# Performance work log

Measured on AMD Instinct MI355X. Metric: run time of the kernel, lower is better.

## Reference

```python
import jax, jax.numpy as jnp
import numpy as np
import math

B, T, D = 2, 2048, 1024
H, HD = 16, 64          # num_heads, head_dim = D // H
ROPE, BASE = 64, 10000.0  # rope covers full head dim
GLOBAL_IDS = jnp.array([2, 3, 4, 5, 6, 7], dtype=jnp.int32)


def setup_inputs() -> dict:
    key = jax.random.key(0)
    k1, k2, k3, k4 = jax.random.split(key, 4)
    x = jax.random.normal(k1, (B, T, D), dtype=jnp.float32)
    input_ids = jax.random.randint(k2, (B, T), 0, 1024, dtype=jnp.int32)
    W_qkv = jax.random.normal(k3, (3 * H * HD, D), dtype=jnp.float32) * 0.02
    b_qkv = jnp.zeros((3 * H * HD,), dtype=jnp.float32)
    W_out = jax.random.normal(k4, (D, H * HD), dtype=jnp.float32) * 0.02
    b_out = jnp.zeros((D,), dtype=jnp.float32)
    return {"x": x, "input_ids": input_ids, "W_qkv": W_qkv, "b_qkv": b_qkv,
            "W_out": W_out, "b_out": b_out}


def _apply_rotary(x, cos, sin):
    # x: [B,H,T,HD]; rope covers first ROPE dims (= full head here)
    x_rot, x_pass = x[..., :ROPE], x[..., ROPE:]
    half = ROPE // 2
    x1, x2 = x_rot[..., :half], x_rot[..., half:]
    x1n = x1 * cos - x2 * sin
    x2n = x1 * sin + x2 * cos
    return jnp.concatenate([x1n, x2n, x_pass], axis=-1)


def reference(x, input_ids, W_qkv, b_qkv, W_out, b_out):
    Bx, Tx, _ = x.shape
    qkv = x @ W_qkv.T + b_qkv                      # [B,T,3*H*HD]
    q, k, v = jnp.split(qkv, 3, axis=-1)
    def heads(t):
        return t.reshape(Bx, Tx, H, HD).transpose(0, 2, 1, 3)  # [B,H,T,HD]
    q, k, v = heads(q), heads(k), heads(v)

    # RoPE
    pos = jnp.arange(Tx, dtype=jnp.float32)
    inv_freq = 1.0 / (BASE ** (jnp.arange(0, ROPE, 2, dtype=jnp.float32) / ROPE))
    freqs = pos[:, None] * inv_freq[None, :]        # [T, ROPE//2]
    cos, sin = jnp.cos(freqs)[None, None], jnp.sin(freqs)[None, None]
    q = _apply_rotary(q, cos, sin)
    k = _apply_rotary(k, cos, sin)

    # causal mask OR global-query rows (BigBird-style)
    causal = jnp.tril(jnp.ones((Tx, Tx), dtype=bool))[None, None]   # [1,1,T,T]
    global_mask = jnp.isin(input_ids, GLOBAL_IDS)                    # [B,T]
    allow = causal | global_mask[:, None, :, None]                   # [B,1,T,T]

    scale = math.sqrt(HD)
    logits = jnp.einsum('bhqd,bhkd->bhqk', q, k) / scale
    neg = -jnp.finfo(logits.dtype).max
    logits = jnp.where(allow, logits, neg)
    attn = jax.nn.softmax(logits, axis=-1)
    out = jnp.einsum('bhqk,bhkd->bhqd', attn, v)
    out = out.transpose(0, 2, 1, 3).reshape(Bx, Tx, H * HD)
    return out @ W_out.T + b_out
```

## Files before the change

### kernel.cpp

```cpp
#include <hip/hip_runtime.h>
#include <math.h>

#define Bc 2
#define Tc 2048
#define Dc 1024
#define Hc 16
#define HDc 64

typedef __attribute__((ext_vector_type(8))) short bf16x8;
typedef __attribute__((ext_vector_type(4))) float f32x4;
typedef __attribute__((ext_vector_type(16))) float f32x16;

__device__ __forceinline__ unsigned short f2bf(float f) {
    union { float f; unsigned int u; } v; v.f = f;
    unsigned int r = (v.u + 0x7FFFu + ((v.u >> 16) & 1u)) >> 16;
    return (unsigned short)r;
}
__device__ __forceinline__ unsigned pack2bf(float a, float b) {
    unsigned au = __float_as_uint(a) + 0x8000u;
    unsigned bu = __float_as_uint(b) + 0x8000u;
    return __builtin_amdgcn_perm(bu, au, 0x07060302u);
}

__device__ __forceinline__ void gload_lds16(const unsigned short* g,
                                            unsigned short* l) {
    __builtin_amdgcn_global_load_lds(
        (const __attribute__((address_space(1))) unsigned int*)g,
        (__attribute__((address_space(3))) unsigned int*)l,
        16, 0, 0);
}

#define CEXP 0.1803368801111204f

__global__ __launch_bounds__(256) void convert_bf16(
    const float* __restrict__ x, const float* __restrict__ wqkv,
    const float* __restrict__ wout,
    unsigned short* __restrict__ xb, unsigned short* __restrict__ wqkvb,
    unsigned short* __restrict__ woutb, float2* __restrict__ ropeTab)
{
    const int gid = blockIdx.x * 256 + threadIdx.x;
    if (gid < Tc * 32) {
        const int t = gid >> 5, i = gid & 31;
        const float freq = exp2f((float)i * -0.4152410118609203f);
        const float ang = (float)t * freq;
        ropeTab[gid] = make_float2(cosf(ang), sinf(ang));
    }
#pragma unroll
    for (int it = 0; it < 4; it++) {
        const int i = (it * 524288 + gid) * 4;
        const float* src; unsigned short* dst; int off;
        if (i < 4194304)      { src = x;    dst = xb;    off = i; }
        else if (i < 7340032) { src = wqkv; dst = wqkvb; off = i - 4194304; }
        else                  { src = wout; dst = woutb; off = i - 7340032; }
        float4 v = *(const float4*)&src[off];
        ushort4 o;
        o.x = f2bf(v.x); o.y = f2bf(v.y); o.z = f2bf(v.z); o.w = f2bf(v.w);
        *(ushort4*)&dst[off] = o;
    }
}

template <int MODE, int MT, int NT>
__global__ __launch_bounds__(256) void gemm_mfma(
    const unsigned short* __restrict__ A, const unsigned short* __restrict__ W,
    const float* __restrict__ bias, float* __restrict__ C,
    unsigned short* __restrict__ Qp, unsigned short* __restrict__ Kp,
    unsigned short* __restrict__ Vtp, const float2* __restrict__ ropeTab,
    int M, int N, int K)
{
    __shared__ unsigned short Apk[MT * 32 * 64];
    __shared__ unsigned short Bpk[NT * 32 * 64];

    const int tid = threadIdx.x;
    const int lane = tid & 63;
    const int wave = tid >> 6;
    const int quad = lane >> 4;
    const int c = lane & 15;
    const int wm = wave >> 1;
    const int wn = wave & 1;

    const int flat = blockIdx.y * gridDim.x + blockIdx.x;
    const int cpx = gridDim.x >> 3;
    const int xcd = flat & 7;
    const int idxq = flat >> 3;
    const int bx = xcd * cpx + (idxq % cpx);
    const int by = idxq / cpx;
    const int m0 = by * (MT * 32);
    const int n0 = bx * (NT * 32);

    f32x4 acc[MT][NT];
#pragma unroll
    for (int mt = 0; mt < MT; mt++)
#pragma unroll
        for (int nt = 0; nt < NT; nt++) acc[mt][nt] = (f32x4){0.f, 0.f, 0.f, 0.f};

    const int lrow = lane >> 3;
    const int srcoct = (lane & 7) ^ lrow;

    for (int k0 = 0; k0 < K; k0 += 64) {
        __syncthreads();
#pragma unroll
        for (int i = 0; i < MT; i++) {
            const int r = wave * (MT * 8) + i * 8 + lrow;
            gload_lds16(&A[(size_t)(m0 + r) * K + k0 + srcoct * 8],
                        &Apk[(wave * MT * 8 + i * 8) * 64]);
        }
#pragma unroll
        for (int i = 0; i < NT; i++) {
            const int r = wave * (NT * 8) + i * 8 + lrow;
            gload_lds16(&W[(size_t)(n0 + r) * K + k0 + srcoct * 8],
                        &Bpk[(wave * NT * 8 + i * 8) * 64]);
        }
        __syncthreads();
#pragma unroll
        for (int ko = 0; ko < 2; ko++) {
            bf16x8 af[MT], bf[NT];
#pragma unroll
            for (int mt = 0; mt < MT; mt++) {
                const int m = wm * (MT * 16) + mt * 16 + c;
                af[mt] = *(const bf16x8*)&Apk[(m * 8 + ((ko * 4 + quad) ^ (m & 7))) * 8];
            }
#pragma unroll
            for (int nt = 0; nt < NT; nt++) {
                const int n = wn * (NT * 16) + nt * 16 + c;
                bf[nt] = *(const bf16x8*)&Bpk[(n * 8 + ((ko * 4 + quad) ^ (n & 7))) * 8];
            }
#pragma unroll
            for (int mt = 0; mt < MT; mt++)
#pragma unroll
                for (int nt = 0; nt < NT; nt++)
                    acc[mt][nt] = __builtin_amdgcn_mfma_f32_16x16x32_bf16(
                        af[mt], bf[nt], acc[mt][nt], 0, 0, 0);
        }
    }

    if (MODE == 0) {
#pragma unroll
        for (int mt = 0; mt < MT; mt++) {
            const int m = m0 + wm * (MT * 16) + mt * 16 + quad * 4;
#pragma unroll
            for (int nt = 0; nt < NT; nt++) {
                const int n = n0 + wn * (NT * 16) + nt * 16 + c;
                const float bv = bias[n];
#pragma unroll
                for (int reg = 0; reg < 4; reg++)
                    C[(size_t)(m + reg) * N + n] = acc[mt][nt][reg] + bv;
            }
        }
    } else {
        const int n_wave = n0 + wn * 64;
        const int which = n_wave >> 10;
        const int h = (n_wave >> 6) & 15;
        const int b = m0 >> 11;
        const int t_base = (m0 & 2047) + wm * 64;

        __syncthreads();
        unsigned short* stg = ((wave < 2) ? Apk : Bpk) + (wave & 1) * 4096;

        if (which < 2) {
            unsigned short* dst = (which == 0) ? Qp : Kp;
#pragma unroll
            for (int mt = 0; mt < 4; mt++) {
#pragma unroll
                for (int nt = 0; nt < 2; nt++) {
                    const int i1 = nt * 16 + c;
                    const float bv1 = bias[n_wave + i1];
                    const float bv2 = bias[n_wave + 32 + i1];
#pragma unroll
                    for (int reg = 0; reg < 4; reg++) {
                        const int row = mt * 16 + quad * 4 + reg;
                        const float2 cs = ropeTab[(t_base + row) * 32 + i1];
                        const float x1 = acc[mt][nt][reg] + bv1;
                        const float x2 = acc[mt][nt + 2][reg] + bv2;
                        const int col2 = 32 + i1;
                        stg[(row * 8 + ((i1 >> 3) ^ (row & 7))) * 8 + (i1 & 7)] =
                            f2bf(x1 * cs.x - x2 * cs.y);
                        stg[(row * 8 + ((col2 >> 3) ^ (row & 7))) * 8 + (col2 & 7)] =
                            f2bf(x1 * cs.y + x2 * cs.x);
                    }
                }
            }
            const size_t obase = ((size_t)(b * Hc + h) * Tc + t_base) * HDc;
            const int oct = lane & 7;
#pragma unroll
            for (int k = 0; k < 8; k++) {
                const int f = lane * 8 + k * 512;
                const int row = f >> 6;
                bf16x8 vv = *(const bf16x8*)&stg[(row * 8 + (oct ^ (row & 7))) * 8];
                *(bf16x8*)&dst[obase + f] = vv;
            }
        } else {
#pragma unroll
            for (int mt = 0; mt < 4; mt++) {
#pragma unroll
                for (int nt = 0; nt < 4; nt++) {
                    const int d = nt * 16 + c;
                    const float bv = bias[n_wave + d];
#pragma unroll
                    for (int reg = 0; reg < 4; reg++) {
                        const int r = mt * 16 + quad * 4 + reg;
                        stg[(d * 8 + ((r >> 3) ^ (d & 7))) * 8 + (r & 7)] =
                            f2bf(acc[mt][nt][reg] + bv);
                    }
                }
            }
            const size_t vbase = (size_t)(b * Hc + h) * HDc * Tc;
            const int oct = lane & 7;
#pragma unroll
            for (int k = 0; k < 8; k++) {
                const int d = (lane >> 3) + k * 8;
                bf16x8 vv = *(const bf16x8*)&stg[(d * 8 + (oct ^ (d & 7))) * 8];
                *(bf16x8*)&Vtp[vbase + (size_t)d * Tc + t_base + oct * 8] = vv;
            }
        }
    }
}

__global__ __launch_bounds__(256, 4) void attn_fused(
    const unsigned short* __restrict__ Q, const unsigned short* __restrict__ K,
    const unsigned short* __restrict__ Vt, const int* __restrict__ ids,
    unsigned short* __restrict__ AO)
{
    __shared__ __align__(16) float smem[8448];

    const int tid = threadIdx.x;
    const int lane = tid & 63;
    const int wave = tid >> 6;
    const int c32 = lane & 31;
    const int h = lane >> 5;
    const int blk = blockIdx.x;

    if (blk < 32) {
        int* s_list = (int*)smem;
        int* s_cnt = (int*)smem + 64;
        float* s_accm = smem + 128;
        float* s_lm = s_accm + 8192;

        const int bh = blk;
        const int b = bh >> 4;
        const int hd = bh & 15;
        const size_t qkbase = (size_t)bh * Tc * HDc;

        if (tid == 0) *s_cnt = 0;
        __syncthreads();
        for (int i = tid; i < Tc; i += 256) {
            int id = ids[b * Tc + i];
            if ((unsigned)(id - 2) <= 5u) {
                int p = atomicAdd(s_cnt, 1);
                if (p < 64) s_list[p] = i;
            }
        }
        __syncthreads();
        const int cnt = min(*s_cnt, 64);

        for (int pass = 0; pass * 32 < cnt; pass++) {
            const int slot = pass * 32 + c32;
            const int row = (slot < cnt) ? s_list[slot] : s_list[0];

            bf16x8 qf[4];
#pragma unroll
            for (int ko = 0; ko < 4; ko++)
                qf[ko] = *(const bf16x8*)&Q[qkbase + (size_t)row * HDc + ko * 16 + h * 8];

            f32x16 acc0 = {}, acc1 = {};
            float lacc = 0.0f;

            for (int it = wave; it < Tc / 64; it += 4) {
                const int t0 = it * 64;
                f32x16 s0 = {}, s1 = {};
#pragma unroll
                for (int ko = 0; ko < 4; ko++) {
                    const int koff = ko * 16 + h * 8;
                    bf16x8 kf0 = *(const bf16x8*)&K[qkbase + (size_t)(t0 + c32) * HDc + koff];
                    bf16x8 kf1 = *(const bf16x8*)&K[qkbase + (size_t)(t0 + 32 + c32) * HDc + koff];
                    s0 = __builtin_amdgcn_mfma_f32_32x32x16_bf16(kf0, qf[ko], s0, 0, 0, 0);
                    s1 = __builtin_amdgcn_mfma_f32_32x32x16_bf16(kf1, qf[ko], s1, 0, 0, 0);
                }
                float v[32];
#pragma unroll
                for (int r = 0; r < 16; r++) { v[r] = s0[r]; v[16 + r] = s1[r]; }
#pragma unroll
                for (int i = 0; i < 32; i++) v[i] = exp2f(v[i] * CEXP);
                unsigned pk[16];
#pragma unroll
                for (int i = 0; i < 16; i++) pk[i] = pack2bf(v[2 * i], v[2 * i + 1]);
#pragma unroll
                for (int st = 1; st < 32; st <<= 1)
#pragma unroll
                    for (int i = 0; i < 32; i += 2 * st) v[i] += v[i + st];
                lacc += v[0];
#pragma unroll
                for (int ko = 0; ko < 4; ko++) {
                    const int a = (ko >> 1) * 8 + (ko & 1) * 4;
                    unsigned keep0 = h ? pk[a + 2] : pk[a + 0];
                    unsigned keep1 = h ? pk[a + 3] : pk[a + 1];
                    unsigned send0 = h ? pk[a + 0] : pk[a + 2];
                    unsigned send1 = h ? pk[a + 1] : pk[a + 3];
                    unsigned recv0 = (unsigned)__shfl_xor((int)send0, 32);
                    unsigned recv1 = (unsigned)__shfl_xor((int)send1, 32);
                    union { bf16x8 v8; unsigned u[4]; } pf;
                    pf.u[0] = h ? recv0 : keep0;
                    pf.u[1] = h ? recv1 : keep1;
                    pf.u[2] = h ? keep0 : recv0;
                    pf.u[3] = h ? keep1 : recv1;
                    const int oct = ko * 2 + h;
                    bf16x8 vf0 = *(const bf16x8*)&Vt[qkbase + (size_t)c32 * Tc + t0 + oct * 8];
                    bf16x8 vf1 = *(const bf16x8*)&Vt[qkbase + (size_t)(32 + c32) * Tc + t0 + oct * 8];
                    acc0 = __builtin_amdgcn_mfma_f32_32x32x16_bf16(vf0, pf.v8, acc0, 0, 0, 0);
                    acc1 = __builtin_amdgcn_mfma_f32_32x32x16_bf16(vf1, pf.v8, acc1, 0, 0, 0);
                }
            }

            const float lfull = lacc + __shfl_xor(lacc, 32);
            if (h == 0) s_lm[wave * 32 + c32] = lfull;
#pragma unroll
            for (int r = 0; r < 16; r++) {
                const int d = (r & 3) + 8 * (r >> 2) + 4 * h;
                s_accm[(wave * 64 + d) * 32 + c32] = acc0[r];
                s_accm[(wave * 64 + 32 + d) * 32 + c32] = acc1[r];
            }
            __syncthreads();
            for (int i = tid; i < 2048; i += 256) {
                const int sl = i >> 6, d = i & 63;
                if (pass * 32 + sl < cnt) {
                    const float o = s_accm[(0 * 64 + d) * 32 + sl] + s_accm[(1 * 64 + d) * 32 + sl] +
                                    s_accm[(2 * 64 + d) * 32 + sl] + s_accm[(3 * 64 + d) * 32 + sl];
                    const float lt = s_lm[sl] + s_lm[32 + sl] + s_lm[64 + sl] + s_lm[96 + sl];
                    const int qrow = s_list[pass * 32 + sl];
                    AO[((size_t)(b * Tc + qrow)) * Dc + hd * HDc + d] = f2bf(o / lt);
                }
            }
            __syncthreads();
        }
        return;
    }

    unsigned short* KV = (unsigned short*)smem;
    unsigned short* Ke = KV;
    unsigned short* Ko = KV + 4096;
    unsigned short* Ve = KV + 8192;
    unsigned short* Vo = KV + 12288;

    const int idx = blk - 32;
    const int bh = (idx & 7) + 8 * ((idx >> 3) & 3);
    const int b = bh >> 4;
    const int hd = bh & 15;
    const int w = idx >> 5;
    const int u = w & 7, tq = w >> 3;
    const int j = (tq == 0) ? u : (tq == 1) ? 31 - u : (tq == 2) ? 8 + u : 23 - u;
    const int qb0 = j * 64;
    const int nT = j + 1;
    const int wq0 = qb0 + (wave & 1) * 32;
    const size_t qkbase = (size_t)bh * Tc * HDc;
    const int q = wq0 + c32;

    bf16x8 qf[4];
#pragma unroll
    for (int ko = 0; ko < 4; ko++)
        qf[ko] = *(const bf16x8*)&Q[qkbase + (size_t)q * HDc + ko * 16 + h * 8];

    const int myid = ids[b * Tc + q];
    const bool gr = ((unsigned)(myid - 2) <= 5u);

    f32x16 acc0 = {}, acc1 = {};
    float lacc = 0.0f;

    const int lrow = lane >> 3;
    const int srcoct = (lane & 7) ^ lrow;
    const int jb = wave * 2;

    auto stageK = [&](int t0, unsigned short* buf) {
#pragma unroll
        for (int i = 0; i < 2; i++) {
            const int jj = jb + i;
            const int row = jj * 8 + lrow;
            gload_lds16(&K[qkbase + (size_t)(t0 + row) * HDc + srcoct * 8],
                        &buf[jj * 512]);
        }
    };
    auto stageV = [&](int t0, unsigned short* buf) {
#pragma unroll
        for (int i = 0; i < 2; i++) {
            const int jj = jb + i;
            const int d = jj * 8 + lrow;
            gload_lds16(&Vt[qkbase + (size_t)d * Tc + t0 + srcoct * 8],
                        &buf[jj * 512]);
        }
    };

    auto computeT = [&](int t0, const unsigned short* Kb, const unsigned short* Vb) {
        f32x16 s0 = {}, s1 = {};
#pragma unroll
        for (int ko = 0; ko < 4; ko++) {
            const int oct = ko * 2 + h;
            const int k0i = c32;
            const int k1i = 32 + c32;
            bf16x8 kf0 = *(const bf16x8*)&Kb[(k0i * 8 + (oct ^ (k0i & 7))) * 8];
            bf16x8 kf1 = *(const bf16x8*)&Kb[(k1i * 8 + (oct ^ (k1i & 7))) * 8];
            s0 = __builtin_amdgcn_mfma_f32_32x32x16_bf16(kf0, qf[ko], s0, 0, 0, 0);
            s1 = __builtin_amdgcn_mfma_f32_32x32x16_bf16(kf1, qf[ko], s1, 0, 0, 0);
        }

        float v[32];
#pragma unroll
        for (int r = 0; r < 16; r++) { v[r] = s0[r]; v[16 + r] = s1[r]; }
#pragma unroll
        for (int i = 0; i < 32; i++) v[i] = exp2f(v[i] * CEXP);

        const bool needMask = (t0 + 63 > wq0);
        if (needMask) {
            const int thr = wq0 + c32 - t0 - 4 * h;
#pragma unroll
            for (int kt = 0; kt < 2; kt++)
#pragma unroll
                for (int r = 0; r < 16; r++) {
                    const int ckr = kt * 32 + (r & 3) + 8 * (r >> 2);
                    v[kt * 16 + r] = (ckr <= thr) ? v[kt * 16 + r] : 0.0f;
                }
        }

        unsigned pk[16];
#pragma unroll
        for (int i = 0; i < 16; i++) pk[i] = pack2bf(v[2 * i], v[2 * i + 1]);

#pragma unroll
        for (int st = 1; st < 32; st <<= 1)
#pragma unroll
            for (int i = 0; i < 32; i += 2 * st) v[i] += v[i + st];
        lacc += v[0];

#pragma unroll
        for (int ko = 0; ko < 4; ko++) {
            const int a = (ko >> 1) * 8 + (ko & 1) * 4;
            unsigned keep0 = h ? pk[a + 2] : pk[a + 0];
            unsigned keep1 = h ? pk[a + 3] : pk[a + 1];
            unsigned send0 = h ? pk[a + 0] : pk[a + 2];
            unsigned send1 = h ? pk[a + 1] : pk[a + 3];
            unsigned recv0 = (unsigned)__shfl_xor((int)send0, 32);
            unsigned recv1 = (unsigned)__shfl_xor((int)send1, 32);
            union { bf16x8 v8; unsigned u[4]; } pf;
            pf.u[0] = h ? recv0 : keep0;
            pf.u[1] = h ? recv1 : keep1;
            pf.u[2] = h ? keep0 : recv0;
            pf.u[3] = h ? keep1 : recv1;
            const int oct = ko * 2 + h;
            const int d0 = c32, d1 = 32 + c32;
            bf16x8 vf0 = *(const bf16x8*)&Vb[(d0 * 8 + (oct ^ (d0 & 7))) * 8];
            bf16x8 vf1 = *(const bf16x8*)&Vb[(d1 * 8 + (oct ^ (d1 & 7))) * 8];
            acc0 = __builtin_amdgcn_mfma_f32_32x32x16_bf16(vf0, pf.v8, acc0, 0, 0, 0);
            acc1 = __builtin_amdgcn_mfma_f32_32x32x16_bf16(vf1, pf.v8, acc1, 0, 0, 0);
        }
    };

    for (int tp = 0; tp < nT; tp += 2) {
        __syncthreads();
        stageK(tp * 64, Ke);
        stageV(tp * 64, Ve);
        const bool has2 = (tp + 1) < nT;
        if (has2) {
            stageK((tp + 1) * 64, Ko);
            stageV((tp + 1) * 64, Vo);
        }
        __syncthreads();
        if ((wave >> 1) == 0) computeT(tp * 64, Ke, Ve);
        else if (has2) computeT((tp + 1) * 64, Ko, Vo);
    }

    __syncthreads();
    float* mrg = smem + (wave & 1) * 2176;
    if (wave >= 2) {
#pragma unroll
        for (int r = 0; r < 16; r++) {
            mrg[r * 64 + lane] = acc0[r];
            mrg[(16 + r) * 64 + lane] = acc1[r];
        }
        mrg[2048 + lane] = lacc;
    }
    __syncthreads();
    if (wave >= 2) return;
#pragma unroll
    for (int r = 0; r < 16; r++) {
        acc0[r] += mrg[r * 64 + lane];
        acc1[r] += mrg[(16 + r) * 64 + lane];
    }
    lacc += mrg[2048 + lane];

    const float l = lacc + __shfl_xor(lacc, 32);
    if (!gr) {
        const float inv = 1.0f / l;
        unsigned short* dst = &AO[((size_t)(b * Tc + q)) * Dc + hd * HDc];
#pragma unroll
        for (int i = 0; i < 8; i++) {
            const int r = 2 * i;
            const int d = (r & 3) + 8 * (r >> 2) + 4 * h;
            *(unsigned*)&dst[d]      = pack2bf(acc0[r] * inv, acc0[r + 1] * inv);
            *(unsigned*)&dst[32 + d] = pack2bf(acc1[r] * inv, acc1[r + 1] * inv);
        }
    }
}

extern "C" void kernel_launch(void* const* d_in, const int* in_sizes, int n_in,
                              void* d_out, int out_size, void* d_ws, size_t ws_size,
                              hipStream_t stream)
{
    const float* x    = (const float*)d_in[0];
    const int*   ids  = (const int*)d_in[1];
    const float* Wqkv = (const float*)d_in[2];
    const float* bqkv = (const float*)d_in[3];
    const float* Wout = (const float*)d_in[4];
    const float* bout = (const float*)d_in[5];
    float* out = (float*)d_out;

    const size_t TEN = (size_t)Bc * Hc * Tc * HDc;
    unsigned short* xb    = (unsigned short*)d_ws;
    unsigned short* wqkvb = xb + 4194304;
    unsigned short* woutb = wqkvb + 3145728;
    float2* ropeTab       = (float2*)(woutb + 1048576);
    unsigned short* Qb    = (unsigned short*)(ropeTab + 65536);
    unsigned short* Kb    = Qb + TEN;
    unsigned short* Vtb   = Kb + TEN;
    unsigned short* AOb   = Vtb + TEN;

    convert_bf16<<<2048, 256, 0, stream>>>(x, Wqkv, Wout, xb, wqkvb, woutb,
                                           ropeTab);
    dim3 g1(3072 / 128, 4096 / 128);
    gemm_mfma<1, 4, 4><<<g1, 256, 0, stream>>>(xb, wqkvb, bqkv, nullptr,
                                               Qb, Kb, Vtb, ropeTab,
                                               4096, 3072, 1024);
    attn_fused<<<1056, 256, 0, stream>>>(Qb, Kb, Vtb, ids, AOb);
    dim3 g4(1024 / 64, 4096 / 64);
    gemm_mfma<0, 2, 2><<<g4, 256, 0, stream>>>(AOb, woutb, bout, out,
                                               nullptr, nullptr, nullptr, nullptr,
                                               4096, 1024, 1024);
}
```

Baseline: 193.5 us.

## Split attention tile into QK and PV phases and prefetch next K during PV

The per-tile attention computation is split into a QK/softmax phase and a PV phase. V loads are issued while QK runs, and the next pair of K tiles is staged into LDS while the PV MFMAs run, so global-to-LDS latency overlaps with compute instead of being exposed behind a barrier. The GEMM kernel also drops its XCD-aware block remapping and uses plain blockIdx tiling, which may change L2 locality. Odd tile counts are handled by re-staging the last tile, which adds a little redundant loading.

```diff
diff --git a/kernel.cpp b/kernel.cpp
--- a/kernel.cpp
+++ b/kernel.cpp
@@ -77,15 +77,8 @@
     const int c = lane & 15;
     const int wm = wave >> 1;
     const int wn = wave & 1;
-
-    const int flat = blockIdx.y * gridDim.x + blockIdx.x;
-    const int cpx = gridDim.x >> 3;
-    const int xcd = flat & 7;
-    const int idxq = flat >> 3;
-    const int bx = xcd * cpx + (idxq % cpx);
-    const int by = idxq / cpx;
-    const int m0 = by * (MT * 32);
-    const int n0 = bx * (NT * 32);
+    const int m0 = blockIdx.y * (MT * 32);
+    const int n0 = blockIdx.x * (NT * 32);
 
     f32x4 acc[MT][NT];
 #pragma unroll
@@ -349,6 +342,7 @@
     const int j = (tq == 0) ? u : (tq == 1) ? 31 - u : (tq == 2) ? 8 + u : 23 - u;
     const int qb0 = j * 64;
     const int nT = j + 1;
+    const int grp = wave >> 1;
     const int wq0 = qb0 + (wave & 1) * 32;
     const size_t qkbase = (size_t)bh * Tc * HDc;
     const int q = wq0 + c32;
@@ -387,7 +381,9 @@
         }
     };
 
-    auto computeT = [&](int t0, const unsigned short* Kb, const unsigned short* Vb) {
+    unsigned pk[16];
+
+    auto qkPhase = [&](int t0, const unsigned short* Kb) {
         f32x16 s0 = {}, s1 = {};
 #pragma unroll
         for (int ko = 0; ko < 4; ko++) {
@@ -418,7 +414,6 @@
                 }
         }
 
-        unsigned pk[16];
 #pragma unroll
         for (int i = 0; i < 16; i++) pk[i] = pack2bf(v[2 * i], v[2 * i + 1]);
 
@@ -427,7 +422,9 @@
 #pragma unroll
             for (int i = 0; i < 32; i += 2 * st) v[i] += v[i + st];
         lacc += v[0];
-
+    };
+
+    auto pvPhase = [&](const unsigned short* Vb) {
 #pragma unroll
         for (int ko = 0; ko < 4; ko++) {
             const int a = (ko >> 1) * 8 + (ko & 1) * 4;
@@ -451,18 +448,25 @@
         }
     };
 
+    {
+        const int t1 = (1 < nT) ? 1 : 0;
+        stageK(0, Ke);
+        stageK(t1 * 64, Ko);
+    }
     for (int tp = 0; tp < nT; tp += 2) {
         __syncthreads();
-        stageK(tp * 64, Ke);
+        const int to = (tp + 1 < nT) ? tp + 1 : tp;
         stageV(tp * 64, Ve);
-        const bool has2 = (tp + 1) < nT;
-        if (has2) {
-            stageK((tp + 1) * 64, Ko);
-            stageV((tp + 1) * 64, Vo);
-        }
-        __syncthreads();
-        if ((wave >> 1) == 0) computeT(tp * 64, Ke, Ve);
-        else if (has2) computeT((tp + 1) * 64, Ko, Vo);
+        stageV(to * 64, Vo);
+        const bool valid = (grp == 0) || (tp + 1 < nT);
+        if (valid) qkPhase(grp ? (tp + 1) * 64 : tp * 64, grp ? Ko : Ke);
+        __syncthreads();
+        if (tp + 2 < nT) {
+            const int t3 = (tp + 3 < nT) ? tp + 3 : tp + 2;
+            stageK((tp + 2) * 64, Ke);
+            stageK(t3 * 64, Ko);
+        }
+        if (valid) pvPhase(grp ? Vo : Ve);
     }
 
     __syncthreads();
```

Result: no change. 192.5 us (-0.5%).
